# Kernel optimization log

Measured on AMD Instinct MI355X. Metric: run time of the kernel, lower is better.

Reference implementation:

```python
import jax, jax.numpy as jnp
import numpy as np

NUM_CLASSES = 80
IOU_EPS = 1e-5


def _corners(b):
    # NormalizeBoxes with default shape=ones((2,)) divides by 1 -> plain corner transform
    cx, cy, w, h = b[..., 0], b[..., 1], b[..., 2], b[..., 3]
    return cy - h / 2, cx - w / 2, cy + h / 2, cx + w / 2  # y1, x1, y2, x2


def _pairwise_iou(gt, pr):
    # gt: [B,G,4], pr: [P,4] -> [B,G,P]
    ga = gt[..., 2] * gt[..., 3]                      # [B,G]
    pa = pr[:, 2] * pr[:, 3]                          # [P]
    gy1, gx1, gy2, gx2 = _corners(gt)                 # [B,G]
    py1, px1, py2, px2 = _corners(pr)                 # [P]
    ih = jnp.maximum(0.0, jnp.minimum(gy2[..., None], py2) - jnp.maximum(gy1[..., None], py1))
    iw = jnp.maximum(0.0, jnp.minimum(gx2[..., None], px2) - jnp.maximum(gx1[..., None], px1))
    inter = iw * ih
    union = ga[..., None] + pa - inter
    return inter / (union + IOU_EPS)


def _assign_boxes(gt_boxes, pr_boxes):
    B, G, _ = gt_boxes.shape
    P = pr_boxes.shape[1]
    gt_labels = gt_boxes[..., -2]                     # [B,G]
    gt_conf = gt_boxes[..., -1]                       # [B,G]
    pr = pr_boxes[0].astype(jnp.float32)              # priors shared across batch: [P,4]

    iou = _pairwise_iou(gt_boxes[..., :4].astype(jnp.float32), pr)  # [B,G,P]
    valid = (gt_boxes[..., 0] != -1.0).astype(iou.dtype)
    iou = iou * valid[..., None]

    # matches: all pairs with iou>=0.5, plus the argmax prior per valid (conf>0) GT.
    thresh = iou >= 0.5                                             # [B,G,P]
    best_p = jnp.argmax(iou, axis=-1)                               # [B,G]
    best = (jnp.arange(P)[None, None, :] == best_p[..., None]) & (gt_conf > 0.0)[..., None]

    # thresh matches then best matches -> best overrides thresh; within each
    g_ids = jnp.arange(G)[None, :, None]
    g_thresh = jnp.max(jnp.where(thresh, g_ids, -1), axis=1)        # [B,P]
    g_best = jnp.max(jnp.where(best, g_ids, -1), axis=1)            # [B,P]
    win_g = jnp.where(g_best >= 0, g_best, g_thresh)                # [B,P]
    matched = win_g >= 0

    labels = jnp.take_along_axis(gt_labels, jnp.maximum(win_g, 0), axis=1)  # [B,P]
    cls_id = jnp.where(matched, labels.astype(jnp.int32), NUM_CLASSES)
    onehot = jax.nn.one_hot(cls_id, NUM_CLASSES + 1, dtype=jnp.float32)     # [B,P,C+1]
    assign_mask = onehot[..., -1]                                           # 1 = background
    ignore = jnp.any((iou < 0.5) & (iou >= 0.4), axis=1)                    # [B,P]
    assign_mask = jnp.where(ignore, -1.0, assign_mask)

    # loc targets: tf.scatter_nd SUMS duplicate indices, so each (b,p) target is the
    # sum of encodings over all its matches (thresh + best, duplicates counted twice).
    w = thresh.astype(jnp.float32) + best.astype(jnp.float32)       # [B,G,P]
    gb = gt_boxes[..., :4].astype(jnp.float32)
    safe_log = lambda v: jnp.where(v > 0, jnp.log(jnp.maximum(v, 1e-20)), 0.0)
    W = jnp.sum(w, axis=1)                                          # [B,P] match counts
    S_cx = jnp.einsum('bgp,bg->bp', w, gb[..., 0])
    S_cy = jnp.einsum('bgp,bg->bp', w, gb[..., 1])
    S_lw = jnp.einsum('bgp,bg->bp', w, safe_log(gb[..., 2]))
    S_lh = jnp.einsum('bgp,bg->bp', w, safe_log(gb[..., 3]))
    p_cx, p_cy, p_w, p_h = pr[:, 0], pr[:, 1], pr[:, 2], pr[:, 3]   # [P]
    hat_cx = (S_cx - W * p_cx) / p_w
    hat_cy = (S_cy - W * p_cy) / p_h
    hat_w = S_lw - W * jnp.log(p_w)
    hat_h = S_lh - W * jnp.log(p_h)
    loc_true = jnp.stack([hat_cx, hat_cy, hat_w, hat_h], axis=2)    # [B,P,4]

    cls_true = onehot[..., :NUM_CLASSES]
    return cls_true, loc_true, assign_mask[..., None]


def setup_inputs() -> dict:
    key = jax.random.key(0)
    ks = jax.random.split(key, 8)
    B, G, P = 8, 64, 32768
    NUM_VALID = 48
    g_cx = jax.random.uniform(ks[0], (B, G), minval=0.05, maxval=0.95)
    g_cy = jax.random.uniform(ks[1], (B, G), minval=0.05, maxval=0.95)
    g_w = jax.random.uniform(ks[2], (B, G), minval=0.02, maxval=0.30)
    g_h = jax.random.uniform(ks[3], (B, G), minval=0.02, maxval=0.30)
    labels = jax.random.randint(ks[4], (B, G), 0, NUM_CLASSES).astype(jnp.float32)
    conf = jnp.ones((B, G), dtype=jnp.float32)
    gt = jnp.stack([g_cx, g_cy, g_w, g_h, labels, conf], axis=-1)
    valid = (jnp.arange(G) < NUM_VALID)[None, :, None]
    gt_boxes = jnp.where(valid, gt, -1.0)  # pad trailing GTs with -1 (conf -1 <= 0)
    p_cx = jax.random.uniform(ks[5], (P,), minval=0.0, maxval=1.0)
    p_cy = jax.random.uniform(ks[6], (P,), minval=0.0, maxval=1.0)
    pwh = jax.random.uniform(ks[7], (P, 2), minval=0.02, maxval=0.30)
    pr = jnp.concatenate([p_cx[:, None], p_cy[:, None], pwh], axis=1)
    pr_boxes = jnp.broadcast_to(pr[None], (B, P, 4))
    return {"gt_boxes": gt_boxes, "pr_boxes": pr_boxes}


def reference(gt_boxes, pr_boxes):
    return _assign_boxes(gt_boxes, pr_boxes)
```

## Files before the change

### kernel.cpp

```cpp
#include <hip/hip_runtime.h>
#include <cmath>

#define NBATCH 8
#define NGT    64
#define NPR    32768
#define NC     80

#define CHUNKS 16
#define CHUNK  (NPR / CHUNKS)
#define GTPB   8

__global__ __launch_bounds__(256) void k_bestp_part(const float* __restrict__ gt,
                                                    const float* __restrict__ pr,
                                                    float* __restrict__ pval,
                                                    int* __restrict__ pidx) {
#pragma clang fp contract(off)
    const int chunk = blockIdx.x;
    const int gg    = blockIdx.y;
    const int tid   = threadIdx.x;

    __shared__ float sy1[GTPB], sx1[GTPB], sy2[GTPB], sx2[GTPB], sga[GTPB];
    __shared__ int   sv[GTPB];
    if (tid < GTPB) {
        const float* g6 = gt + ((size_t)gg * GTPB + tid) * 6;
        float cx = g6[0], cy = g6[1], w = g6[2], h = g6[3];
        sy1[tid] = cy - h * 0.5f;
        sx1[tid] = cx - w * 0.5f;
        sy2[tid] = cy + h * 0.5f;
        sx2[tid] = cx + w * 0.5f;
        sga[tid] = w * h;
        sv[tid]  = (cx != -1.0f) ? 1 : 0;
    }
    __syncthreads();

    float gy1[GTPB], gx1[GTPB], gy2[GTPB], gx2[GTPB], ga[GTPB];
    int   gv[GTPB];
    #pragma unroll
    for (int j = 0; j < GTPB; ++j) {
        gy1[j] = sy1[j]; gx1[j] = sx1[j]; gy2[j] = sy2[j]; gx2[j] = sx2[j];
        ga[j] = sga[j]; gv[j] = sv[j];
    }

    float best[GTPB]; int bi[GTPB];
    #pragma unroll
    for (int j = 0; j < GTPB; ++j) { best[j] = -1.0f; bi[j] = 0; }

    const int base = chunk * CHUNK;
    #pragma unroll 4
    for (int k = 0; k < CHUNK / 256; ++k) {
        int p = base + k * 256 + tid;
        float4 pv = ((const float4*)pr)[p];
        float py1 = pv.y - pv.w * 0.5f;
        float px1 = pv.x - pv.z * 0.5f;
        float py2 = pv.y + pv.w * 0.5f;
        float px2 = pv.x + pv.z * 0.5f;
        float pa  = pv.z * pv.w;
        #pragma unroll
        for (int j = 0; j < GTPB; ++j) {
            float ih = fmaxf(0.0f, fminf(gy2[j], py2) - fmaxf(gy1[j], py1));
            float iw = fmaxf(0.0f, fminf(gx2[j], px2) - fmaxf(gx1[j], px1));
            float inter = iw * ih;
            float uni   = ga[j] + pa - inter;
            float iou   = inter / (uni + 1e-5f);
            iou = gv[j] ? iou : 0.0f;
            if (iou > best[j]) { best[j] = iou; bi[j] = p; }
        }
    }

    #pragma unroll
    for (int j = 0; j < GTPB; ++j) {
        #pragma unroll
        for (int off = 32; off > 0; off >>= 1) {
            float ov = __shfl_down(best[j], off);
            int   oi = __shfl_down(bi[j], off);
            if (ov > best[j] || (ov == best[j] && oi < bi[j])) {
                best[j] = ov; bi[j] = oi;
            }
        }
    }

    __shared__ float rv[4][GTPB];
    __shared__ int   rix[4][GTPB];
    const int wave = tid >> 6;
    if ((tid & 63) == 0) {
        #pragma unroll
        for (int j = 0; j < GTPB; ++j) { rv[wave][j] = best[j]; rix[wave][j] = bi[j]; }
    }
    __syncthreads();
    if (tid < GTPB) {
        float v = rv[0][tid]; int i = rix[0][tid];
        #pragma unroll
        for (int w = 1; w < 4; ++w) {
            float v2 = rv[w][tid]; int i2 = rix[w][tid];
            if (v2 > v || (v2 == v && i2 < i)) { v = v2; i = i2; }
        }
        int bg = gg * GTPB + tid;
        pval[bg * CHUNKS + chunk] = v;
        pidx[bg * CHUNKS + chunk] = i;
    }
}

__global__ __launch_bounds__(256) void k_finish(const float* __restrict__ gt,
                                                const float* __restrict__ pval,
                                                const int* __restrict__ pidx,
                                                float* __restrict__ prep) {
#pragma clang fp contract(off)
    const int bg = blockIdx.x * 256 + threadIdx.x;
    if (bg >= NBATCH * NGT) return;
    const float* g6 = gt + (size_t)bg * 6;
    float cx = g6[0], cy = g6[1], w = g6[2], h = g6[3], lab = g6[4], conf = g6[5];
    bool valid = (cx != -1.0f);
    float y1 = cy - h * 0.5f;
    float x1 = cx - w * 0.5f;
    float y2 = cy + h * 0.5f;
    float x2 = cx + w * 0.5f;
    if (!valid) { y1 = 3e38f; y2 = 3e38f; }
    float ga = w * h;
    float lw = (w > 0.0f) ? logf(fmaxf(w, 1e-20f)) : 0.0f;
    float lh = (h > 0.0f) ? logf(fmaxf(h, 1e-20f)) : 0.0f;

    float v = pval[bg * CHUNKS + 0]; int i = pidx[bg * CHUNKS + 0];
    #pragma unroll
    for (int c = 1; c < CHUNKS; ++c) {
        float v2 = pval[bg * CHUNKS + c]; int i2 = pidx[bg * CHUNKS + c];
        if (v2 > v || (v2 == v && i2 < i)) { v = v2; i = i2; }
    }
    int bp = (conf > 0.0f) ? i : -1;

    float4* q = (float4*)prep + (size_t)bg * 3;
    q[0] = make_float4(y1, x1, y2, x2);
    q[1] = make_float4(ga, cx, cy, lab);
    q[2] = make_float4(lw, lh, __int_as_float(bp), 0.0f);
}

__global__ __launch_bounds__(256) void k_assign(const float* __restrict__ pr,
                                                const float* __restrict__ prep,
                                                float* __restrict__ out_cls,
                                                float* __restrict__ out_loc,
                                                float* __restrict__ out_msk) {
#pragma clang fp contract(off)
    const int b   = blockIdx.y;
    const int tid = threadIdx.x;
    const int p   = blockIdx.x * 256 + tid;

    const float4* __restrict__ q = (const float4*)prep + (size_t)b * NGT * 3;

    float4 pv = ((const float4*)pr)[p];
    const float px = pv.x, py = pv.y, pw = pv.z, ph = pv.w;
    const float py1 = py - ph * 0.5f;
    const float px1 = px - pw * 0.5f;
    const float py2 = py + ph * 0.5f;
    const float px2 = px + pw * 0.5f;
    const float pa  = pw * ph;

    int  g_th = -1, g_bs = -1;
    bool ignore = false;
    float W = 0.0f, Scx = 0.0f, Scy = 0.0f, Slw = 0.0f, Slh = 0.0f;

    #pragma unroll 8
    for (int g = 0; g < NGT; ++g) {
        float4 q0 = q[3 * g + 0];
        float4 q1 = q[3 * g + 1];
        float4 q2 = q[3 * g + 2];
        float ih = fmaxf(0.0f, fminf(q0.z, py2) - fmaxf(q0.x, py1));
        float iw = fmaxf(0.0f, fminf(q0.w, px2) - fmaxf(q0.y, px1));
        float inter = iw * ih;
        float uni   = q1.x + pa - inter;
        float iou   = inter / (uni + 1e-5f);
        bool th = (iou >= 0.5f);
        bool bs = (__float_as_int(q2.z) == p);
        if (th) g_th = g;
        if (bs) g_bs = g;
        ignore = ignore || (iou < 0.5f && iou >= 0.4f);
        float wg = (float)th + (float)bs;
        W   += wg;
        Scx += wg * q1.y;
        Scy += wg * q1.z;
        Slw += wg * q2.x;
        Slh += wg * q2.y;
    }

    const int  win     = (g_bs >= 0) ? g_bs : g_th;
    const bool matched = (win >= 0);
    float labf = prep[((size_t)b * NGT + (win >= 0 ? win : 0)) * 12 + 7];
    const int cls = matched ? (int)labf : NC;
    float msk = matched ? 0.0f : 1.0f;
    if (ignore) msk = -1.0f;

    const float hcx = (Scx - W * px) / pw;
    const float hcy = (Scy - W * py) / ph;
    const float hw  = Slw - W * logf(pw);
    const float hh  = Slh - W * logf(ph);

    const size_t bp_i = (size_t)b * NPR + p;
    ((float4*)out_loc)[bp_i] = make_float4(hcx, hcy, hw, hh);
    out_msk[bp_i] = msk;

    __shared__ int s_cls[256];
    s_cls[tid] = cls;
    __syncthreads();
    const size_t base4 = ((size_t)b * NPR + (size_t)blockIdx.x * 256) * NC / 4;
    float4* oc4 = (float4*)out_cls;
    #pragma unroll
    for (int k = 0; k < (256 * NC / 4) / 256; ++k) {
        int idx = tid + k * 256;
        int e0  = idx * 4;
        int pl  = e0 / NC;
        int c0  = e0 - pl * NC;
        int cl  = s_cls[pl];
        float4 v;
        v.x = (c0     == cl) ? 1.0f : 0.0f;
        v.y = (c0 + 1 == cl) ? 1.0f : 0.0f;
        v.z = (c0 + 2 == cl) ? 1.0f : 0.0f;
        v.w = (c0 + 3 == cl) ? 1.0f : 0.0f;
        oc4[base4 + idx] = v;
    }
}

extern "C" void kernel_launch(void* const* d_in, const int* in_sizes, int n_in,
                              void* d_out, int out_size, void* d_ws, size_t ws_size,
                              hipStream_t stream) {
    const float* gt = (const float*)d_in[0];
    const float* pr = (const float*)d_in[1];

    float* pval = (float*)d_ws;
    int*   pidx = (int*)((char*)d_ws + 32 * 1024);
    float* prep = (float*)((char*)d_ws + 64 * 1024);

    float* out_cls = (float*)d_out;
    float* out_loc = out_cls + (size_t)NBATCH * NPR * NC;
    float* out_msk = out_loc + (size_t)NBATCH * NPR * 4;

    dim3 g1(CHUNKS, NBATCH * NGT / GTPB);
    k_bestp_part<<<g1, 256, 0, stream>>>(gt, pr, pval, pidx);

    k_finish<<<(NBATCH * NGT + 255) / 256, 256, 0, stream>>>(gt, pval, pidx, prep);

    dim3 g2(NPR / 256, NBATCH);
    k_assign<<<g2, 256, 0, stream>>>(pr, prep, out_cls, out_loc, out_msk);
}
```

Before: 135.7 us.

## Stage GT table in LDS, assign two priors per thread, nontemporal one-hot stores

The assign kernel now copies the per-batch GT table into shared memory once per block and processes two priors per thread, which reuses each GT load across both. The grid shrinks to match. The large one-hot class output is written with nontemporal stores to cut cache pollution on a store-bandwidth-bound write. In exchange there are fewer blocks, more registers per thread, and an extra barrier.

```diff
diff --git a/kernel.cpp b/kernel.cpp
--- a/kernel.cpp
+++ b/kernel.cpp
@@ -9,6 +9,10 @@
 #define CHUNKS 16
 #define CHUNK  (NPR / CHUNKS)
 #define GTPB   8
+#define APT    2
+#define APB    (256 * APT)
+
+typedef float v4f __attribute__((ext_vector_type(4)));
 
 __global__ __launch_bounds__(256) void k_bestp_part(const float* __restrict__ gt,
                                                     const float* __restrict__ pr,
@@ -141,79 +145,98 @@
 #pragma clang fp contract(off)
     const int b   = blockIdx.y;
     const int tid = threadIdx.x;
-    const int p   = blockIdx.x * 256 + tid;
-
-    const float4* __restrict__ q = (const float4*)prep + (size_t)b * NGT * 3;
-
-    float4 pv = ((const float4*)pr)[p];
-    const float px = pv.x, py = pv.y, pw = pv.z, ph = pv.w;
-    const float py1 = py - ph * 0.5f;
-    const float px1 = px - pw * 0.5f;
-    const float py2 = py + ph * 0.5f;
-    const float px2 = px + pw * 0.5f;
-    const float pa  = pw * ph;
-
-    int  g_th = -1, g_bs = -1;
-    bool ignore = false;
-    float W = 0.0f, Scx = 0.0f, Scy = 0.0f, Slw = 0.0f, Slh = 0.0f;
-
-    #pragma unroll 8
+    const int p0  = blockIdx.x * APB + tid;
+
+    __shared__ float4 sq[NGT * 3];
+    __shared__ int    s_cls[APB];
+    if (tid < NGT * 3) sq[tid] = ((const float4*)prep)[(size_t)b * NGT * 3 + tid];
+    __syncthreads();
+
+    float px[APT], py[APT], pw[APT], ph[APT];
+    float py1[APT], px1[APT], py2[APT], px2[APT], pa[APT];
+    #pragma unroll
+    for (int a = 0; a < APT; ++a) {
+        float4 pv = ((const float4*)pr)[p0 + a * 256];
+        px[a] = pv.x; py[a] = pv.y; pw[a] = pv.z; ph[a] = pv.w;
+        py1[a] = pv.y - pv.w * 0.5f;
+        px1[a] = pv.x - pv.z * 0.5f;
+        py2[a] = pv.y + pv.w * 0.5f;
+        px2[a] = pv.x + pv.z * 0.5f;
+        pa[a]  = pv.z * pv.w;
+    }
+
+    int  g_th[APT], g_bs[APT];
+    bool ign[APT];
+    float W[APT], Scx[APT], Scy[APT], Slw[APT], Slh[APT];
+    #pragma unroll
+    for (int a = 0; a < APT; ++a) {
+        g_th[a] = -1; g_bs[a] = -1; ign[a] = false;
+        W[a] = 0.0f; Scx[a] = 0.0f; Scy[a] = 0.0f; Slw[a] = 0.0f; Slh[a] = 0.0f;
+    }
+
+    #pragma unroll 4
     for (int g = 0; g < NGT; ++g) {
-        float4 q0 = q[3 * g + 0];
-        float4 q1 = q[3 * g + 1];
-        float4 q2 = q[3 * g + 2];
-        float ih = fmaxf(0.0f, fminf(q0.z, py2) - fmaxf(q0.x, py1));
-        float iw = fmaxf(0.0f, fminf(q0.w, px2) - fmaxf(q0.y, px1));
-        float inter = iw * ih;
-        float uni   = q1.x + pa - inter;
-        float iou   = inter / (uni + 1e-5f);
-        bool th = (iou >= 0.5f);
-        bool bs = (__float_as_int(q2.z) == p);
-        if (th) g_th = g;
-        if (bs) g_bs = g;
-        ignore = ignore || (iou < 0.5f && iou >= 0.4f);
-        float wg = (float)th + (float)bs;
-        W   += wg;
-        Scx += wg * q1.y;
-        Scy += wg * q1.z;
-        Slw += wg * q2.x;
-        Slh += wg * q2.y;
-    }
-
-    const int  win     = (g_bs >= 0) ? g_bs : g_th;
-    const bool matched = (win >= 0);
-    float labf = prep[((size_t)b * NGT + (win >= 0 ? win : 0)) * 12 + 7];
-    const int cls = matched ? (int)labf : NC;
-    float msk = matched ? 0.0f : 1.0f;
-    if (ignore) msk = -1.0f;
-
-    const float hcx = (Scx - W * px) / pw;
-    const float hcy = (Scy - W * py) / ph;
-    const float hw  = Slw - W * logf(pw);
-    const float hh  = Slh - W * logf(ph);
-
-    const size_t bp_i = (size_t)b * NPR + p;
-    ((float4*)out_loc)[bp_i] = make_float4(hcx, hcy, hw, hh);
-    out_msk[bp_i] = msk;
-
-    __shared__ int s_cls[256];
-    s_cls[tid] = cls;
-    __syncthreads();
-    const size_t base4 = ((size_t)b * NPR + (size_t)blockIdx.x * 256) * NC / 4;
-    float4* oc4 = (float4*)out_cls;
-    #pragma unroll
-    for (int k = 0; k < (256 * NC / 4) / 256; ++k) {
+        float4 q0 = sq[3 * g + 0];
+        float4 q1 = sq[3 * g + 1];
+        float4 q2 = sq[3 * g + 2];
+        int bp = __float_as_int(q2.z);
+        #pragma unroll
+        for (int a = 0; a < APT; ++a) {
+            float ih = fmaxf(0.0f, fminf(q0.z, py2[a]) - fmaxf(q0.x, py1[a]));
+            float iw = fmaxf(0.0f, fminf(q0.w, px2[a]) - fmaxf(q0.y, px1[a]));
+            float inter = iw * ih;
+            float uni   = q1.x + pa[a] - inter;
+            float iou   = inter / (uni + 1e-5f);
+            bool th = (iou >= 0.5f);
+            bool bs = (bp == p0 + a * 256);
+            if (th) g_th[a] = g;
+            if (bs) g_bs[a] = g;
+            ign[a] = ign[a] || (iou < 0.5f && iou >= 0.4f);
+            float wg = (float)th + (float)bs;
+            W[a]   += wg;
+            Scx[a] += wg * q1.y;
+            Scy[a] += wg * q1.z;
+            Slw[a] += wg * q2.x;
+            Slh[a] += wg * q2.y;
+        }
+    }
+
+    #pragma unroll
+    for (int a = 0; a < APT; ++a) {
+        const int  win     = (g_bs[a] >= 0) ? g_bs[a] : g_th[a];
+        const bool matched = (win >= 0);
+        float labf = sq[3 * (matched ? win : 0) + 1].w;
+        const int cls = matched ? (int)labf : NC;
+        float msk = matched ? 0.0f : 1.0f;
+        if (ign[a]) msk = -1.0f;
+
+        const float hcx = (Scx[a] - W[a] * px[a]) / pw[a];
+        const float hcy = (Scy[a] - W[a] * py[a]) / ph[a];
+        const float hw  = Slw[a] - W[a] * logf(pw[a]);
+        const float hh  = Slh[a] - W[a] * logf(ph[a]);
+
+        const size_t bp_i = (size_t)b * NPR + p0 + a * 256;
+        ((float4*)out_loc)[bp_i] = make_float4(hcx, hcy, hw, hh);
+        out_msk[bp_i] = msk;
+        s_cls[tid + a * 256] = cls;
+    }
+    __syncthreads();
+
+    const size_t base4 = ((size_t)b * NPR + (size_t)blockIdx.x * APB) * NC / 4;
+    v4f* oc4 = (v4f*)out_cls;
+    #pragma unroll
+    for (int k = 0; k < (APB * NC / 4) / 256; ++k) {
         int idx = tid + k * 256;
         int e0  = idx * 4;
         int pl  = e0 / NC;
         int c0  = e0 - pl * NC;
         int cl  = s_cls[pl];
-        float4 v;
+        v4f v;
         v.x = (c0     == cl) ? 1.0f : 0.0f;
         v.y = (c0 + 1 == cl) ? 1.0f : 0.0f;
         v.z = (c0 + 2 == cl) ? 1.0f : 0.0f;
         v.w = (c0 + 3 == cl) ? 1.0f : 0.0f;
-        oc4[base4 + idx] = v;
+        __builtin_nontemporal_store(v, &oc4[base4 + idx]);
     }
 }
 
@@ -236,6 +259,6 @@
 
     k_finish<<<(NBATCH * NGT + 255) / 256, 256, 0, stream>>>(gt, pval, pidx, prep);
 
-    dim3 g2(NPR / 256, NBATCH);
+    dim3 g2(NPR / APB, NBATCH);
     k_assign<<<g2, 256, 0, stream>>>(pr, prep, out_cls, out_loc, out_msk);
 }
```

After: 139.7 us. +3.0%, slower.
